# Kernel optimization log

Measured on AMD Instinct MI355X. Metric: run time of the kernel, lower is better.

The kernel has to match this reference:

```python
import jax, jax.numpy as jnp
import numpy as np

N = 30000      # nodes
E = 480000     # edges (avg degree 16)
NF = 4         # n_field
NM = 8         # n_meshfield
H = 128        # hidden_size == latent_size
T = 4          # n_time
DEPTH_MID = 8  # depth-2 middle convs per GCNBlock
EPS = 1e-5     # PyG InstanceNorm eps
DT = 5 * (4.0 / 200)  # = 0.1, hard-coded in forward


def _glorot(k, shape):
    fan_in = shape[-2]
    return (jax.random.uniform(k, shape, jnp.float32, -1.0, 1.0) / np.sqrt(fan_in)).astype(jnp.float32)


def setup_inputs() -> dict:
    key = jax.random.key(0)
    ks = jax.random.split(key, 12)
    inp = {}
    inp['F_0'] = jax.random.normal(ks[0], (N, NF), jnp.float32)
    inp['edge_index'] = jax.random.randint(ks[1], (2, E), 0, N)
    inp['meshfield'] = jax.random.normal(ks[2], (N, NM), jnp.float32)
    inp['n_time'] = T
    # mesh_decriptor GCNBlock params (10 GCNConv layers)
    inp['mesh_W0'] = _glorot(ks[3], (NM, H)); inp['mesh_b0'] = jnp.zeros((H,), jnp.float32)
    inp['mesh_Wh'] = _glorot(ks[4], (DEPTH_MID, H, H)); inp['mesh_bh'] = jnp.zeros((DEPTH_MID, H), jnp.float32)
    inp['mesh_W9'] = _glorot(ks[5], (H, H)); inp['mesh_b9'] = jnp.zeros((H,), jnp.float32)
    # differentiator GCNBlock params; input dim = n_field + latent_size
    din = NF + H
    inp['diff_W0'] = _glorot(ks[6], (din, H)); inp['diff_b0'] = jnp.zeros((H,), jnp.float32)
    inp['diff_Wh'] = _glorot(ks[7], (DEPTH_MID, H, H)); inp['diff_bh'] = jnp.zeros((DEPTH_MID, H), jnp.float32)
    inp['diff_W9'] = _glorot(ks[8], (H, NF)); inp['diff_b9'] = jnp.zeros((NF,), jnp.float32)
    return inp


def _gcn_norm(edge_index, n):
    # PyG GCNConv: add self-loops, sym-normalize D^-1/2 (A+I) D^-1/2
    loops = jnp.arange(n)
    row = jnp.concatenate([edge_index[0], loops])
    col = jnp.concatenate([edge_index[1], loops])
    deg = jax.ops.segment_sum(jnp.ones_like(col, jnp.float32), col, num_segments=n)
    dinv = jnp.where(deg > 0, jax.lax.rsqrt(jnp.maximum(deg, 1.0)), 0.0)
    return row, col, dinv[row] * dinv[col]


def _conv(x, W, b, row, col, enorm, n):
    h = x @ W                                   # [n, out]
    m = h[row] * enorm[:, None]                 # gather + edge normalization
    return jax.ops.segment_sum(m, col, num_segments=n) + b  # scatter-add + bias


def _instance_norm(x):
    # single graph, affine=False: per-channel normalize over nodes
    m = x.mean(axis=0)
    v = x.var(axis=0)
    return (x - m) * jax.lax.rsqrt(v + EPS)


def _gcn_block(x, W0, b0, Wh, bh, W9, b9, row, col, enorm, n):
    x = _conv(x, W0, b0, row, col, enorm, n)
    x = _instance_norm(x)
    def body(c, wb):
        W, b = wb
        return _conv(jax.nn.relu(c), W, b, row, col, enorm, n), None
    x, _ = jax.lax.scan(body, x, (Wh, bh))
    return _conv(x, W9, b9, row, col, enorm, n)


def reference(F_0, edge_index, meshfield, n_time,
              mesh_W0, mesh_b0, mesh_Wh, mesh_bh, mesh_W9, mesh_b9,
              diff_W0, diff_b0, diff_Wh, diff_bh, diff_W9, diff_b9):
    n = F_0.shape[0]
    row, col, enorm = _gcn_norm(edge_index, n)
    mesh = jnp.tanh(_gcn_block(meshfield, mesh_W0, mesh_b0, mesh_Wh, mesh_bh,
                               mesh_W9, mesh_b9, row, col, enorm, n))

    def step(F_cur, _):
        x = jnp.concatenate([F_cur, mesh], axis=1)   # [n, n_field + latent]
        F_dot = jnp.tanh(_gcn_block(x, diff_W0, diff_b0, diff_Wh, diff_bh,
                                    diff_W9, diff_b9, row, col, enorm, n))
        F_next = jnp.tanh(F_cur + F_dot * DT)
        # original: F_current = F_next.detach()
        return jax.lax.stop_gradient(F_next), (F_next, F_dot)

    _, (Fs, F_dots) = jax.lax.scan(step, F_0, None, length=n_time)
    # [T, n, f] -> [n, T, f] to match torch.cat(..., dim=1)
    return jnp.transpose(Fs, (1, 0, 2)), jnp.transpose(F_dots, (1, 0, 2))
```

## Files before the change

kernel.cpp:

```cpp
#include <hip/hip_runtime.h>
#include <math.h>

typedef __attribute__((ext_vector_type(8))) short short8;
typedef __attribute__((ext_vector_type(4))) float f32x4;
typedef unsigned int uint;
typedef unsigned short ushort;

__device__ __forceinline__ ushort f2bf(float f) {
  union { float f; uint u; } v; v.f = f;
  uint u = v.u;
  uint r = (u + 0x7FFFu + ((u >> 16) & 1u)) >> 16;
  return (ushort)r;
}
__device__ __forceinline__ float bflo(uint u) { union { uint u; float f; } v; v.u = u << 16; return v.f; }
__device__ __forceinline__ float bfhi(uint u) { union { uint u; float f; } v; v.u = u & 0xFFFF0000u; return v.f; }
__device__ __forceinline__ uint packbf(float a, float b) { return (uint)f2bf(a) | ((uint)f2bf(b) << 16); }


static __global__ void k_count(const int* __restrict__ col, int* __restrict__ cnt, int E) {
  int e = blockIdx.x * blockDim.x + threadIdx.x;
  if (e < E) atomicAdd(&cnt[col[e]], 1);
}

static __global__ void k_dinv(const int* __restrict__ cnt, float* __restrict__ dinv, int N) {
  int v = blockIdx.x * blockDim.x + threadIdx.x;
  if (v < N) dinv[v] = rsqrtf((float)cnt[v] + 1.0f);
}

static __global__ __launch_bounds__(1024) void k_scan(const int* __restrict__ cnt,
                                                      int* __restrict__ rowptr, int N) {
  const int t = threadIdx.x;
  const int per = (N + 1023) / 1024;
  int lo = t * per, hi = min(lo + per, N);
  if (lo > N) lo = N;
  if (hi < lo) hi = lo;
  int sum = 0;
  for (int i = lo; i < hi; ++i) sum += cnt[i];
  int lane = t & 63, w = t >> 6;
  int v = sum;
#pragma unroll
  for (int d = 1; d < 64; d <<= 1) {
    int u = __shfl_up(v, d, 64);
    if (lane >= d) v += u;
  }
  __shared__ int wsum[16];
  if (lane == 63) wsum[w] = v;
  __syncthreads();
  if (t < 16) {
    int x = wsum[t];
#pragma unroll
    for (int d = 1; d < 16; d <<= 1) {
      int u = __shfl_up(x, d, 64);
      if (t >= d) x += u;
    }
    wsum[t] = x;
  }
  __syncthreads();
  int base = (w ? wsum[w - 1] : 0) + v - sum;
  int run = base;
  for (int i = lo; i < hi; ++i) { rowptr[i] = run; run += cnt[i]; }
  if (t == 1023) rowptr[N] = run;
}

static __global__ void k_fill(const int* __restrict__ row, const int* __restrict__ col,
                              const float* __restrict__ dinv, const int* __restrict__ rowptr,
                              int* __restrict__ fillc, int* __restrict__ csr_src,
                              float* __restrict__ csr_w, int E) {
  int e = blockIdx.x * blockDim.x + threadIdx.x;
  if (e >= E) return;
  int s = row[e], d = col[e];
  int pos = rowptr[d] + atomicAdd(&fillc[d], 1);
  csr_src[pos] = s;
  csr_w[pos] = dinv[s] * dinv[d];
}


static __global__ void k_wprep(const float* __restrict__ W, ushort* __restrict__ Wt,
                               int K, int Kpad, int Nc) {
  int l = blockIdx.y;
  int idx = blockIdx.x * 256 + threadIdx.x;
  if (idx >= Nc * Kpad) return;
  int n = idx / Kpad, k = idx - n * Kpad;
  const float* Wl = W + (size_t)l * K * Nc;
  ushort* Wtl = Wt + (size_t)l * Nc * Kpad;
  Wtl[idx] = (k < K) ? f2bf(Wl[(size_t)k * Nc + n]) : (ushort)0;
}


static __global__ __launch_bounds__(256) void k_gemm16(
    const ushort* __restrict__ A, const ushort* __restrict__ Bt,
    int K, const float* __restrict__ bias,
    float* __restrict__ outF, ushort* __restrict__ outB,
    int M) {
  __shared__ ushort As[128 * 40];
  __shared__ ushort Bs[128 * 40];
  const int tid = threadIdx.x;
  const int lane = tid & 63;
  const int wave = tid >> 6;
  const int wr = wave >> 1, wc = wave & 1;
  const int bm = blockIdx.x * 128;
  const int l15 = lane & 15, lk = lane >> 4;
  const int r0 = tid >> 2, o0 = tid & 3;

  f32x4 acc[4][4];
#pragma unroll
  for (int i = 0; i < 4; ++i)
#pragma unroll
    for (int j = 0; j < 4; ++j) acc[i][j] = (f32x4){0.f, 0.f, 0.f, 0.f};

  for (int k0 = 0; k0 < K; k0 += 32) {
    short8 a0 = *(const short8*)(A + (size_t)(bm + r0) * K + k0 + o0 * 8);
    short8 a1 = *(const short8*)(A + (size_t)(bm + r0 + 64) * K + k0 + o0 * 8);
    short8 b0 = *(const short8*)(Bt + (size_t)r0 * K + k0 + o0 * 8);
    short8 b1 = *(const short8*)(Bt + (size_t)(r0 + 64) * K + k0 + o0 * 8);
    __syncthreads();
    *(short8*)(As + r0 * 40 + o0 * 8) = a0;
    *(short8*)(As + (r0 + 64) * 40 + o0 * 8) = a1;
    *(short8*)(Bs + r0 * 40 + o0 * 8) = b0;
    *(short8*)(Bs + (r0 + 64) * 40 + o0 * 8) = b1;
    __syncthreads();
    short8 af[4], bfr[4];
#pragma unroll
    for (int i = 0; i < 4; ++i) {
      af[i]  = *(const short8*)(As + (wr * 64 + i * 16 + l15) * 40 + lk * 8);
      bfr[i] = *(const short8*)(Bs + (wc * 64 + i * 16 + l15) * 40 + lk * 8);
    }
#pragma unroll
    for (int i = 0; i < 4; ++i)
#pragma unroll
      for (int j = 0; j < 4; ++j)
        acc[i][j] = __builtin_amdgcn_mfma_f32_16x16x32_bf16(af[i], bfr[j], acc[i][j], 0, 0, 0);
  }
#pragma unroll
  for (int i = 0; i < 4; ++i) {
#pragma unroll
    for (int r = 0; r < 4; ++r) {
      int row = bm + wr * 64 + i * 16 + lk * 4 + r;
      if (row >= M) continue;
#pragma unroll
      for (int j = 0; j < 4; ++j) {
        int col = wc * 64 + j * 16 + l15;
        float v = acc[i][j][r] + (bias ? bias[col] : 0.f);
        if (outF) outF[(size_t)row * 128 + col] = v;
        if (outB) outB[(size_t)row * 128 + col] = f2bf(v);
      }
    }
  }
}


static __global__ __launch_bounds__(256) void k_gemm_small(
    const ushort* __restrict__ A, const float* __restrict__ W, float* __restrict__ Y, int M) {
  __shared__ float Ws[512];
  int tid = threadIdx.x;
  for (int i = tid; i < 512; i += 256) Ws[i] = W[i];
  __syncthreads();
  int m = blockIdx.x * 256 + tid;
  if (m >= M) return;
  const uint* a = (const uint*)(A + (size_t)m * 128);
  float a0 = 0, a1 = 0, a2 = 0, a3 = 0;
#pragma unroll 8
  for (int k2 = 0; k2 < 64; ++k2) {
    uint u = a[k2];
    float x0 = bflo(u), x1 = bfhi(u);
    const float* w = Ws + k2 * 8;
    a0 += x0 * w[0] + x1 * w[4];
    a1 += x0 * w[1] + x1 * w[5];
    a2 += x0 * w[2] + x1 * w[6];
    a3 += x0 * w[3] + x1 * w[7];
  }
  float* y = Y + (size_t)m * 4;
  y[0] = a0; y[1] = a1; y[2] = a2; y[3] = a3;
}


static __global__ __launch_bounds__(256) void k_agg16(
    const ushort* __restrict__ Hm, const int* __restrict__ rowptr,
    const int* __restrict__ csr_src, const float* __restrict__ csr_w,
    const float* __restrict__ dinv, const float* __restrict__ bias,
    float* __restrict__ outF,
    ushort* __restrict__ outB, int actB,
    int N) {
  int node = blockIdx.x * 8 + (threadIdx.x >> 5);
  if (node >= N) return;
  int lane = threadIdx.x & 31;
  const uint2* __restrict__ Hu = (const uint2*)Hm;
  float dv = dinv[node];
  float w = dv * dv;
  uint2 su = Hu[(size_t)node * 32 + lane];
  float a0 = w * bflo(su.x), a1 = w * bfhi(su.x);
  float a2 = w * bflo(su.y), a3 = w * bfhi(su.y);
  int s = rowptr[node], e = rowptr[node + 1];
  int i = s;
  for (; i + 8 <= e; i += 8) {
    int s0 = csr_src[i], s1 = csr_src[i + 1], s2 = csr_src[i + 2], s3 = csr_src[i + 3];
    int s4 = csr_src[i + 4], s5 = csr_src[i + 5], s6 = csr_src[i + 6], s7 = csr_src[i + 7];
    float w0 = csr_w[i], w1 = csr_w[i + 1], w2 = csr_w[i + 2], w3 = csr_w[i + 3];
    float w4 = csr_w[i + 4], w5 = csr_w[i + 5], w6 = csr_w[i + 6], w7 = csr_w[i + 7];
    uint2 u0 = Hu[(size_t)s0 * 32 + lane];
    uint2 u1 = Hu[(size_t)s1 * 32 + lane];
    uint2 u2 = Hu[(size_t)s2 * 32 + lane];
    uint2 u3 = Hu[(size_t)s3 * 32 + lane];
    uint2 u4 = Hu[(size_t)s4 * 32 + lane];
    uint2 u5 = Hu[(size_t)s5 * 32 + lane];
    uint2 u6 = Hu[(size_t)s6 * 32 + lane];
    uint2 u7 = Hu[(size_t)s7 * 32 + lane];
    a0 += w0 * bflo(u0.x) + w1 * bflo(u1.x) + w2 * bflo(u2.x) + w3 * bflo(u3.x)
        + w4 * bflo(u4.x) + w5 * bflo(u5.x) + w6 * bflo(u6.x) + w7 * bflo(u7.x);
    a1 += w0 * bfhi(u0.x) + w1 * bfhi(u1.x) + w2 * bfhi(u2.x) + w3 * bfhi(u3.x)
        + w4 * bfhi(u4.x) + w5 * bfhi(u5.x) + w6 * bfhi(u6.x) + w7 * bfhi(u7.x);
    a2 += w0 * bflo(u0.y) + w1 * bflo(u1.y) + w2 * bflo(u2.y) + w3 * bflo(u3.y)
        + w4 * bflo(u4.y) + w5 * bflo(u5.y) + w6 * bflo(u6.y) + w7 * bflo(u7.y);
    a3 += w0 * bfhi(u0.y) + w1 * bfhi(u1.y) + w2 * bfhi(u2.y) + w3 * bfhi(u3.y)
        + w4 * bfhi(u4.y) + w5 * bfhi(u5.y) + w6 * bfhi(u6.y) + w7 * bfhi(u7.y);
  }
  for (; i + 4 <= e; i += 4) {
    int s0 = csr_src[i], s1 = csr_src[i + 1], s2 = csr_src[i + 2], s3 = csr_src[i + 3];
    float w0 = csr_w[i], w1 = csr_w[i + 1], w2 = csr_w[i + 2], w3 = csr_w[i + 3];
    uint2 u0 = Hu[(size_t)s0 * 32 + lane];
    uint2 u1 = Hu[(size_t)s1 * 32 + lane];
    uint2 u2 = Hu[(size_t)s2 * 32 + lane];
    uint2 u3 = Hu[(size_t)s3 * 32 + lane];
    a0 += w0 * bflo(u0.x) + w1 * bflo(u1.x) + w2 * bflo(u2.x) + w3 * bflo(u3.x);
    a1 += w0 * bfhi(u0.x) + w1 * bfhi(u1.x) + w2 * bfhi(u2.x) + w3 * bfhi(u3.x);
    a2 += w0 * bflo(u0.y) + w1 * bflo(u1.y) + w2 * bflo(u2.y) + w3 * bflo(u3.y);
    a3 += w0 * bfhi(u0.y) + w1 * bfhi(u1.y) + w2 * bfhi(u2.y) + w3 * bfhi(u3.y);
  }
  for (; i < e; ++i) {
    int s0 = csr_src[i];
    float w0 = csr_w[i];
    uint2 u0 = Hu[(size_t)s0 * 32 + lane];
    a0 += w0 * bflo(u0.x);
    a1 += w0 * bfhi(u0.x);
    a2 += w0 * bflo(u0.y);
    a3 += w0 * bfhi(u0.y);
  }
  if (bias) {
    float4 bb = *(const float4*)(bias + lane * 4);
    a0 += bb.x; a1 += bb.y; a2 += bb.z; a3 += bb.w;
  }
  if (outF) {
    *(float4*)(outF + (size_t)node * 128 + lane * 4) = make_float4(a0, a1, a2, a3);
  }
  if (outB) {
    float o0 = a0, o1 = a1, o2 = a2, o3 = a3;
    if (actB == 1) {
      o0 = fmaxf(o0, 0.f); o1 = fmaxf(o1, 0.f); o2 = fmaxf(o2, 0.f); o3 = fmaxf(o3, 0.f);
    } else if (actB == 2) {
      o0 = tanhf(o0); o1 = tanhf(o1); o2 = tanhf(o2); o3 = tanhf(o3);
    }
    uint2 ov;
    ov.x = packbf(o0, o1);
    ov.y = packbf(o2, o3);
    ((uint2*)outB)[(size_t)node * 32 + lane] = ov;
  }
}


static __global__ void k_aggF(const float* __restrict__ F, const int* __restrict__ rowptr,
                              const int* __restrict__ csr_src, const float* __restrict__ csr_w,
                              const float* __restrict__ dinv, ushort* __restrict__ AggF16, int N) {
  int idx = blockIdx.x * blockDim.x + threadIdx.x;
  if (idx >= N * 2) return;
  int v = idx >> 1, pr = idx & 1;
  float dv = dinv[v];
  float2 x = *(const float2*)(F + (size_t)v * 4 + pr * 2);
  float a0 = dv * dv * x.x, a1 = dv * dv * x.y;
  int s = rowptr[v], e = rowptr[v + 1];
  for (int i = s; i < e; ++i) {
    float2 xs = *(const float2*)(F + (size_t)csr_src[i] * 4 + pr * 2);
    float w = csr_w[i];
    a0 += w * xs.x;
    a1 += w * xs.y;
  }
  ((uint*)AggF16)[idx] = packbf(a0, a1);
}


static __global__ void k_concat160(const ushort* __restrict__ AggF16,
                                   const ushort* __restrict__ AggMesh16,
                                   ushort* __restrict__ C160, int N) {
  int idx = blockIdx.x * blockDim.x + threadIdx.x;
  if (idx >= N * 80) return;
  int v = idx / 80, j = idx - v * 80;
  uint val = 0;
  if (j < 2) val = ((const uint*)AggF16)[(size_t)v * 2 + j];
  else if (j < 66) val = ((const uint*)AggMesh16)[(size_t)v * 64 + (j - 2)];
  ((uint*)C160)[idx] = val;
}


static __global__ void k_agg_f32(const float* __restrict__ Hm, float* __restrict__ Y,
                                 const int* __restrict__ rowptr, const int* __restrict__ csr_src,
                                 const float* __restrict__ csr_w, const float* __restrict__ dinv,
                                 const float* __restrict__ bias, int N, int C) {
  int idx = blockIdx.x * blockDim.x + threadIdx.x;
  if (idx >= N * C) return;
  int v = idx / C, c = idx - v * C;
  float dv = dinv[v];
  float acc = dv * dv * Hm[(size_t)v * C + c];
  int s = rowptr[v], e = rowptr[v + 1];
  for (int i = s; i < e; ++i) acc += csr_w[i] * Hm[(size_t)csr_src[i] * C + c];
  Y[idx] = acc + bias[c];
}


static __global__ __launch_bounds__(256) void k_in_part(const float* __restrict__ X,
                                                        float* __restrict__ partial, int N) {
  int tid = threadIdx.x;
  int c4 = (tid & 31) * 4;
  int rsub = tid >> 5;
  int row0 = blockIdx.x * 512 + rsub;
  int rowEnd = min(blockIdx.x * 512 + 512, N);
  float s0 = 0, s1 = 0, s2 = 0, s3 = 0, q0 = 0, q1 = 0, q2 = 0, q3 = 0;
  for (int r = row0; r < rowEnd; r += 8) {
    float4 v = *(const float4*)(X + (size_t)r * 128 + c4);
    s0 += v.x; s1 += v.y; s2 += v.z; s3 += v.w;
    q0 += v.x * v.x; q1 += v.y * v.y; q2 += v.z * v.z; q3 += v.w * v.w;
  }
  __shared__ float sb[8][132], qb[8][132];
  sb[rsub][c4] = s0; sb[rsub][c4 + 1] = s1; sb[rsub][c4 + 2] = s2; sb[rsub][c4 + 3] = s3;
  qb[rsub][c4] = q0; qb[rsub][c4 + 1] = q1; qb[rsub][c4 + 2] = q2; qb[rsub][c4 + 3] = q3;
  __syncthreads();
  if (tid < 128) {
    float ss = 0, qq = 0;
#pragma unroll
    for (int g = 0; g < 8; ++g) { ss += sb[g][tid]; qq += qb[g][tid]; }
    partial[(size_t)blockIdx.x * 256 + tid] = ss;
    partial[(size_t)blockIdx.x * 256 + 128 + tid] = qq;
  }
}

static __global__ void k_in_fin(const float* __restrict__ partial, int NB,
                                float* __restrict__ meanv, float* __restrict__ scalev, int N) {
  int c = threadIdx.x;
  if (c >= 128) return;
  float s = 0, q = 0;
  for (int b = 0; b < NB; ++b) {
    s += partial[(size_t)b * 256 + c];
    q += partial[(size_t)b * 256 + 128 + c];
  }
  float m = s / (float)N;
  float var = q / (float)N - m * m;
  meanv[c] = m;
  scalev[c] = rsqrtf(var + 1e-5f);
}

static __global__ void k_in_apply(const float* __restrict__ X, const float* __restrict__ meanv,
                                  const float* __restrict__ scalev, ushort* __restrict__ outB, int N) {
  int idx = blockIdx.x * blockDim.x + threadIdx.x;
  if (idx >= N * 64) return;
  int c2 = idx & 63;
  float2 x = *(const float2*)(X + (size_t)idx * 2);
  float2 mm = *(const float2*)(meanv + c2 * 2);
  float2 sc = *(const float2*)(scalev + c2 * 2);
  float o0 = fmaxf((x.x - mm.x) * sc.x, 0.f);
  float o1 = fmaxf((x.y - mm.y) * sc.y, 0.f);
  ((uint*)outB)[idx] = packbf(o0, o1);
}


static __global__ void k_cast_mesh0(const float* __restrict__ MF, ushort* __restrict__ C32, int N) {
  int idx = blockIdx.x * blockDim.x + threadIdx.x;
  if (idx >= N * 16) return;
  int v = idx >> 4, c2 = idx & 15;
  int c = c2 * 2;
  float x0 = 0.f, x1 = 0.f;
  if (c < 8) { x0 = MF[v * 8 + c]; x1 = MF[v * 8 + c + 1]; }
  ((uint*)C32)[idx] = packbf(x0, x1);
}

static __global__ void k_copy(const float* __restrict__ A, float* __restrict__ B, int n) {
  int i = blockIdx.x * blockDim.x + threadIdx.x;
  if (i < n) B[i] = A[i];
}

static __global__ void k_step_finish(const float* __restrict__ fdot_pre,
                                     const float* __restrict__ Fcur, float* __restrict__ Fnext,
                                     float* __restrict__ out, int N, int T, int t) {
  int idx = blockIdx.x * blockDim.x + threadIdx.x;
  if (idx >= N * 4) return;
  int v = idx >> 2, f = idx & 3;
  float fd = tanhf(fdot_pre[idx]);
  float fn = tanhf(Fcur[idx] + fd * 0.1f);
  Fnext[idx] = fn;
  out[((size_t)v * T + t) * 4 + f] = fn;
  out[(size_t)N * T * 4 + ((size_t)v * T + t) * 4 + f] = fd;
}


extern "C" void kernel_launch(void* const* d_in, const int* in_sizes, int n_in,
                              void* d_out, int out_size, void* d_ws, size_t ws_size,
                              hipStream_t stream) {
  const float* F0        = (const float*)d_in[0];
  const int*   ei        = (const int*)d_in[1];
  const float* meshfield = (const float*)d_in[2];
  const float* mesh_W0 = (const float*)d_in[4];
  const float* mesh_b0 = (const float*)d_in[5];
  const float* mesh_Wh = (const float*)d_in[6];
  const float* mesh_bh = (const float*)d_in[7];
  const float* mesh_W9 = (const float*)d_in[8];
  const float* mesh_b9 = (const float*)d_in[9];
  const float* diff_W0 = (const float*)d_in[10];
  const float* diff_b0 = (const float*)d_in[11];
  const float* diff_Wh = (const float*)d_in[12];
  const float* diff_bh = (const float*)d_in[13];
  const float* diff_W9 = (const float*)d_in[14];
  const float* diff_b9 = (const float*)d_in[15];

  const int N = in_sizes[0] / 4;
  const int E = in_sizes[1] / 2;
  const int H = in_sizes[5];
  const int T = out_size / (N * 4 * 2);
  const int DEPTH = in_sizes[7] / H;
  const int Mpad = (N + 127) / 128 * 128;
  const int NB_IN = (N + 511) / 512;

  const int* erow = ei;
  const int* ecol = ei + E;

  char* p = (char*)d_ws;
  auto alloc = [&](size_t bytes) { char* r = p; p += (bytes + 255) & ~(size_t)255; return r; };
  float* dinv     = (float*)alloc((size_t)N * 4);
  float* X        = (float*)alloc((size_t)N * H * 4);
  ushort* C32     = (ushort*)alloc((size_t)Mpad * 32 * 2);
  ushort* C160    = (ushort*)alloc((size_t)Mpad * 160 * 2);
  ushort* X16a    = (ushort*)alloc((size_t)Mpad * 128 * 2);
  ushort* X16b    = (ushort*)alloc((size_t)Mpad * 128 * 2);
  ushort* Msg16   = (ushort*)alloc((size_t)Mpad * 128 * 2);
  ushort* meshL16 = (ushort*)alloc((size_t)Mpad * 128 * 2);
  ushort* AggM16  = (ushort*)alloc((size_t)Mpad * 128 * 2);
  ushort* AggF16  = (ushort*)alloc((size_t)Mpad * 4 * 2);
  float* msg4     = (float*)alloc((size_t)N * 4 * 4);
  float* fdotp    = (float*)alloc((size_t)N * 4 * 4);
  float* fcur0    = (float*)alloc((size_t)N * 4 * 4);
  float* fcur1    = (float*)alloc((size_t)N * 4 * 4);
  float* partial  = (float*)alloc((size_t)NB_IN * 256 * 4);
  float* meanv    = (float*)alloc(128 * 4);
  float* scalev   = (float*)alloc(128 * 4);
  ushort* W0t_m   = (ushort*)alloc((size_t)128 * 32 * 2);
  ushort* Wht_m   = (ushort*)alloc((size_t)DEPTH * 128 * 128 * 2);
  ushort* W9t_m   = (ushort*)alloc((size_t)128 * 128 * 2);
  ushort* W0t_d   = (ushort*)alloc((size_t)128 * 160 * 2);
  ushort* Wht_d   = (ushort*)alloc((size_t)DEPTH * 128 * 128 * 2);
  float* csr_w    = (float*)alloc((size_t)E * 4);
  int* cnt        = (int*)alloc((size_t)N * 4);
  int* rowptr     = (int*)alloc((size_t)(N + 1) * 4);
  int* fillc      = (int*)alloc((size_t)N * 4);
  int* csr_src    = (int*)alloc((size_t)E * 4);

  {
    dim3 g0((128 * 32 + 255) / 256, 1);
    k_wprep<<<g0, 256, 0, stream>>>(mesh_W0, W0t_m, 8, 32, 128);
    dim3 gh((128 * 128 + 255) / 256, DEPTH);
    k_wprep<<<gh, 256, 0, stream>>>(mesh_Wh, Wht_m, 128, 128, 128);
    dim3 g9((128 * 128 + 255) / 256, 1);
    k_wprep<<<g9, 256, 0, stream>>>(mesh_W9, W9t_m, 128, 128, 128);
    dim3 gd((128 * 160 + 255) / 256, 1);
    k_wprep<<<gd, 256, 0, stream>>>(diff_W0, W0t_d, 132, 160, 128);
    k_wprep<<<gh, 256, 0, stream>>>(diff_Wh, Wht_d, 128, 128, 128);
  }

  hipMemsetAsync(cnt, 0, (size_t)N * 4, stream);
  hipMemsetAsync(fillc, 0, (size_t)N * 4, stream);
  k_count<<<(E + 255) / 256, 256, 0, stream>>>(ecol, cnt, E);
  k_dinv<<<(N + 255) / 256, 256, 0, stream>>>(cnt, dinv, N);
  k_scan<<<1, 1024, 0, stream>>>(cnt, rowptr, N);
  k_fill<<<(E + 255) / 256, 256, 0, stream>>>(erow, ecol, dinv, rowptr, fillc, csr_src, csr_w, E);

  auto gemm = [&](const ushort* A, const ushort* Bt, int K, const float* bias,
                  float* oF, ushort* oB) {
    k_gemm16<<<Mpad / 128, 256, 0, stream>>>(A, Bt, K, bias, oF, oB, N);
  };
  auto agg = [&](const ushort* Hm, const float* bias, float* oF, ushort* oB, int actB) {
    k_agg16<<<(N + 7) / 8, 256, 0, stream>>>(Hm, rowptr, csr_src, csr_w, dinv, bias,
                                             oF, oB, actB, N);
  };
  auto instnorm = [&]() {
    k_in_part<<<NB_IN, 256, 0, stream>>>(X, partial, N);
    k_in_fin<<<1, 128, 0, stream>>>(partial, NB_IN, meanv, scalev, N);
    k_in_apply<<<(N * 64 + 255) / 256, 256, 0, stream>>>(X, meanv, scalev, X16a, N);
  };

  k_cast_mesh0<<<(N * 16 + 255) / 256, 256, 0, stream>>>(meshfield, C32, N);
  gemm(C32, W0t_m, 32, nullptr, nullptr, Msg16);
  agg(Msg16, mesh_b0, X, nullptr, 0);
  instnorm();
  {
    ushort* cur = X16a; ushort* nxt = X16b;
    for (int i = 0; i < DEPTH; ++i) {
      gemm(cur, Wht_m + (size_t)i * 128 * 128, 128, nullptr, nullptr, Msg16);
      agg(Msg16, mesh_bh + (size_t)i * H, nullptr, nxt, (i < DEPTH - 1) ? 1 : 0);
      ushort* tmp = cur; cur = nxt; nxt = tmp;
    }
    gemm(cur, W9t_m, 128, nullptr, nullptr, Msg16);
    agg(Msg16, mesh_b9, nullptr, meshL16, 2 );
  }
  agg(meshL16, nullptr, nullptr, AggM16, 0);

  k_copy<<<(N * 4 + 255) / 256, 256, 0, stream>>>(F0, fcur0, N * 4);
  float* fc = fcur0;
  float* fn = fcur1;
  float* out = (float*)d_out;

  for (int t = 0; t < T; ++t) {
    k_aggF<<<(N * 2 + 255) / 256, 256, 0, stream>>>(fc, rowptr, csr_src, csr_w, dinv, AggF16, N);
    k_concat160<<<(N * 80 + 255) / 256, 256, 0, stream>>>(AggF16, AggM16, C160, N);
    gemm(C160, W0t_d, 160, diff_b0, X, nullptr);
    instnorm();
    ushort* cur = X16a; ushort* nxt = X16b;
    for (int i = 0; i < DEPTH; ++i) {
      gemm(cur, Wht_d + (size_t)i * 128 * 128, 128, nullptr, nullptr, Msg16);
      agg(Msg16, diff_bh + (size_t)i * H, nullptr, nxt, (i < DEPTH - 1) ? 1 : 0);
      ushort* tmp = cur; cur = nxt; nxt = tmp;
    }
    k_gemm_small<<<(N + 255) / 256, 256, 0, stream>>>(cur, diff_W9, msg4, N);
    k_agg_f32<<<(N * 4 + 255) / 256, 256, 0, stream>>>(msg4, fdotp, rowptr, csr_src, csr_w,
                                                       dinv, diff_b9, N, 4);
    k_step_finish<<<(N * 4 + 255) / 256, 256, 0, stream>>>(fdotp, fc, fn, out, N, T, t);
    float* tmp = fc; fc = fn; fn = tmp;
  }
}
```

Measured before the change: 2.182 ms.

## Fuse instance-norm stats into GEMM epilogue, widen aggregation loads, drop concat kernel

The first differentiator GEMM now accumulates per-column sum and sum-of-squares into a global stats buffer with atomics, replacing the separate partial-reduction and finalize kernels. The apply kernel computes mean and scale itself. The aggregation kernel switches to 16 lanes per node with 16-byte loads and drops the 4-edge unrolled path. The per-step concat kernel is removed: the static mesh part of C160 is built once and aggF writes its columns directly. Float atomics make the statistics nondeterministic in summation order and add a memset per step.

```diff
diff --git a/kernel.cpp b/kernel.cpp
--- a/kernel.cpp
+++ b/kernel.cpp
@@ -91,6 +91,7 @@
     const ushort* __restrict__ A, const ushort* __restrict__ Bt,
     int K, const float* __restrict__ bias,
     float* __restrict__ outF, ushort* __restrict__ outB,
+    float* __restrict__ statac,
     int M) {
   __shared__ ushort As[128 * 40];
   __shared__ ushort Bs[128 * 40];
@@ -144,6 +145,35 @@
         if (outF) outF[(size_t)row * 128 + col] = v;
         if (outB) outB[(size_t)row * 128 + col] = f2bf(v);
       }
+    }
+  }
+  if (statac) {
+    __syncthreads();
+    float* sums = (float*)As;
+    for (int ii = tid; ii < 256; ii += 256) sums[ii] = 0.f;
+    __syncthreads();
+#pragma unroll
+    for (int j = 0; j < 4; ++j) {
+      int col = wc * 64 + j * 16 + l15;
+      float s = 0.f, q = 0.f;
+#pragma unroll
+      for (int i = 0; i < 4; ++i) {
+#pragma unroll
+        for (int r = 0; r < 4; ++r) {
+          int row = bm + wr * 64 + i * 16 + lk * 4 + r;
+          if (row < M) {
+            float v = acc[i][j][r] + (bias ? bias[col] : 0.f);
+            s += v; q += v * v;
+          }
+        }
+      }
+      atomicAdd(&sums[col], s);
+      atomicAdd(&sums[128 + col], q);
+    }
+    __syncthreads();
+    if (tid < 128) {
+      atomicAdd(&statac[tid], sums[tid]);
+      atomicAdd(&statac[128 + tid], sums[128 + tid]);
     }
   }
 }
@@ -181,15 +211,17 @@
     float* __restrict__ outF,
     ushort* __restrict__ outB, int actB,
     int N) {
-  int node = blockIdx.x * 8 + (threadIdx.x >> 5);
+  int node = blockIdx.x * 16 + (threadIdx.x >> 4);
   if (node >= N) return;
-  int lane = threadIdx.x & 31;
-  const uint2* __restrict__ Hu = (const uint2*)Hm;
+  int lane = threadIdx.x & 15;
+  const uint4* __restrict__ Hq = (const uint4*)Hm;
   float dv = dinv[node];
   float w = dv * dv;
-  uint2 su = Hu[(size_t)node * 32 + lane];
+  uint4 su = Hq[(size_t)node * 16 + lane];
   float a0 = w * bflo(su.x), a1 = w * bfhi(su.x);
   float a2 = w * bflo(su.y), a3 = w * bfhi(su.y);
+  float a4 = w * bflo(su.z), a5 = w * bfhi(su.z);
+  float a6 = w * bflo(su.w), a7 = w * bfhi(su.w);
   int s = rowptr[node], e = rowptr[node + 1];
   int i = s;
   for (; i + 8 <= e; i += 8) {
@@ -197,14 +229,14 @@
     int s4 = csr_src[i + 4], s5 = csr_src[i + 5], s6 = csr_src[i + 6], s7 = csr_src[i + 7];
     float w0 = csr_w[i], w1 = csr_w[i + 1], w2 = csr_w[i + 2], w3 = csr_w[i + 3];
     float w4 = csr_w[i + 4], w5 = csr_w[i + 5], w6 = csr_w[i + 6], w7 = csr_w[i + 7];
-    uint2 u0 = Hu[(size_t)s0 * 32 + lane];
-    uint2 u1 = Hu[(size_t)s1 * 32 + lane];
-    uint2 u2 = Hu[(size_t)s2 * 32 + lane];
-    uint2 u3 = Hu[(size_t)s3 * 32 + lane];
-    uint2 u4 = Hu[(size_t)s4 * 32 + lane];
-    uint2 u5 = Hu[(size_t)s5 * 32 + lane];
-    uint2 u6 = Hu[(size_t)s6 * 32 + lane];
-    uint2 u7 = Hu[(size_t)s7 * 32 + lane];
+    uint4 u0 = Hq[(size_t)s0 * 16 + lane];
+    uint4 u1 = Hq[(size_t)s1 * 16 + lane];
+    uint4 u2 = Hq[(size_t)s2 * 16 + lane];
+    uint4 u3 = Hq[(size_t)s3 * 16 + lane];
+    uint4 u4 = Hq[(size_t)s4 * 16 + lane];
+    uint4 u5 = Hq[(size_t)s5 * 16 + lane];
+    uint4 u6 = Hq[(size_t)s6 * 16 + lane];
+    uint4 u7 = Hq[(size_t)s7 * 16 + lane];
     a0 += w0 * bflo(u0.x) + w1 * bflo(u1.x) + w2 * bflo(u2.x) + w3 * bflo(u3.x)
         + w4 * bflo(u4.x) + w5 * bflo(u5.x) + w6 * bflo(u6.x) + w7 * bflo(u7.x);
     a1 += w0 * bfhi(u0.x) + w1 * bfhi(u1.x) + w2 * bfhi(u2.x) + w3 * bfhi(u3.x)
@@ -213,53 +245,54 @@
         + w4 * bflo(u4.y) + w5 * bflo(u5.y) + w6 * bflo(u6.y) + w7 * bflo(u7.y);
     a3 += w0 * bfhi(u0.y) + w1 * bfhi(u1.y) + w2 * bfhi(u2.y) + w3 * bfhi(u3.y)
         + w4 * bfhi(u4.y) + w5 * bfhi(u5.y) + w6 * bfhi(u6.y) + w7 * bfhi(u7.y);
-  }
-  for (; i + 4 <= e; i += 4) {
-    int s0 = csr_src[i], s1 = csr_src[i + 1], s2 = csr_src[i + 2], s3 = csr_src[i + 3];
-    float w0 = csr_w[i], w1 = csr_w[i + 1], w2 = csr_w[i + 2], w3 = csr_w[i + 3];
-    uint2 u0 = Hu[(size_t)s0 * 32 + lane];
-    uint2 u1 = Hu[(size_t)s1 * 32 + lane];
-    uint2 u2 = Hu[(size_t)s2 * 32 + lane];
-    uint2 u3 = Hu[(size_t)s3 * 32 + lane];
-    a0 += w0 * bflo(u0.x) + w1 * bflo(u1.x) + w2 * bflo(u2.x) + w3 * bflo(u3.x);
-    a1 += w0 * bfhi(u0.x) + w1 * bfhi(u1.x) + w2 * bfhi(u2.x) + w3 * bfhi(u3.x);
-    a2 += w0 * bflo(u0.y) + w1 * bflo(u1.y) + w2 * bflo(u2.y) + w3 * bflo(u3.y);
-    a3 += w0 * bfhi(u0.y) + w1 * bfhi(u1.y) + w2 * bfhi(u2.y) + w3 * bfhi(u3.y);
+    a4 += w0 * bflo(u0.z) + w1 * bflo(u1.z) + w2 * bflo(u2.z) + w3 * bflo(u3.z)
+        + w4 * bflo(u4.z) + w5 * bflo(u5.z) + w6 * bflo(u6.z) + w7 * bflo(u7.z);
+    a5 += w0 * bfhi(u0.z) + w1 * bfhi(u1.z) + w2 * bfhi(u2.z) + w3 * bfhi(u3.z)
+        + w4 * bfhi(u4.z) + w5 * bfhi(u5.z) + w6 * bfhi(u6.z) + w7 * bfhi(u7.z);
+    a6 += w0 * bflo(u0.w) + w1 * bflo(u1.w) + w2 * bflo(u2.w) + w3 * bflo(u3.w)
+        + w4 * bflo(u4.w) + w5 * bflo(u5.w) + w6 * bflo(u6.w) + w7 * bflo(u7.w);
+    a7 += w0 * bfhi(u0.w) + w1 * bfhi(u1.w) + w2 * bfhi(u2.w) + w3 * bfhi(u3.w)
+        + w4 * bfhi(u4.w) + w5 * bfhi(u5.w) + w6 * bfhi(u6.w) + w7 * bfhi(u7.w);
   }
   for (; i < e; ++i) {
     int s0 = csr_src[i];
     float w0 = csr_w[i];
-    uint2 u0 = Hu[(size_t)s0 * 32 + lane];
-    a0 += w0 * bflo(u0.x);
-    a1 += w0 * bfhi(u0.x);
-    a2 += w0 * bflo(u0.y);
-    a3 += w0 * bfhi(u0.y);
+    uint4 u0 = Hq[(size_t)s0 * 16 + lane];
+    a0 += w0 * bflo(u0.x); a1 += w0 * bfhi(u0.x);
+    a2 += w0 * bflo(u0.y); a3 += w0 * bfhi(u0.y);
+    a4 += w0 * bflo(u0.z); a5 += w0 * bfhi(u0.z);
+    a6 += w0 * bflo(u0.w); a7 += w0 * bfhi(u0.w);
   }
   if (bias) {
-    float4 bb = *(const float4*)(bias + lane * 4);
-    a0 += bb.x; a1 += bb.y; a2 += bb.z; a3 += bb.w;
+    float4 b0 = *(const float4*)(bias + lane * 8);
+    float4 b1 = *(const float4*)(bias + lane * 8 + 4);
+    a0 += b0.x; a1 += b0.y; a2 += b0.z; a3 += b0.w;
+    a4 += b1.x; a5 += b1.y; a6 += b1.z; a7 += b1.w;
   }
   if (outF) {
-    *(float4*)(outF + (size_t)node * 128 + lane * 4) = make_float4(a0, a1, a2, a3);
+    *(float4*)(outF + (size_t)node * 128 + lane * 8)     = make_float4(a0, a1, a2, a3);
+    *(float4*)(outF + (size_t)node * 128 + lane * 8 + 4) = make_float4(a4, a5, a6, a7);
   }
   if (outB) {
-    float o0 = a0, o1 = a1, o2 = a2, o3 = a3;
+    float o0 = a0, o1 = a1, o2 = a2, o3 = a3, o4 = a4, o5 = a5, o6 = a6, o7 = a7;
     if (actB == 1) {
       o0 = fmaxf(o0, 0.f); o1 = fmaxf(o1, 0.f); o2 = fmaxf(o2, 0.f); o3 = fmaxf(o3, 0.f);
+      o4 = fmaxf(o4, 0.f); o5 = fmaxf(o5, 0.f); o6 = fmaxf(o6, 0.f); o7 = fmaxf(o7, 0.f);
     } else if (actB == 2) {
       o0 = tanhf(o0); o1 = tanhf(o1); o2 = tanhf(o2); o3 = tanhf(o3);
-    }
-    uint2 ov;
-    ov.x = packbf(o0, o1);
-    ov.y = packbf(o2, o3);
-    ((uint2*)outB)[(size_t)node * 32 + lane] = ov;
+      o4 = tanhf(o4); o5 = tanhf(o5); o6 = tanhf(o6); o7 = tanhf(o7);
+    }
+    uint4 ov;
+    ov.x = packbf(o0, o1); ov.y = packbf(o2, o3);
+    ov.z = packbf(o4, o5); ov.w = packbf(o6, o7);
+    ((uint4*)outB)[(size_t)node * 16 + lane] = ov;
   }
 }
 
 
 static __global__ void k_aggF(const float* __restrict__ F, const int* __restrict__ rowptr,
                               const int* __restrict__ csr_src, const float* __restrict__ csr_w,
-                              const float* __restrict__ dinv, ushort* __restrict__ AggF16, int N) {
+                              const float* __restrict__ dinv, ushort* __restrict__ C160, int N) {
   int idx = blockIdx.x * blockDim.x + threadIdx.x;
   if (idx >= N * 2) return;
   int v = idx >> 1, pr = idx & 1;
@@ -273,19 +306,17 @@
     a0 += w * xs.x;
     a1 += w * xs.y;
   }
-  ((uint*)AggF16)[idx] = packbf(a0, a1);
-}
-
-
-static __global__ void k_concat160(const ushort* __restrict__ AggF16,
-                                   const ushort* __restrict__ AggMesh16,
-                                   ushort* __restrict__ C160, int N) {
+  ((uint*)C160)[(size_t)v * 80 + pr] = packbf(a0, a1);
+}
+
+
+static __global__ void k_buildC160(const ushort* __restrict__ AggMesh16,
+                                   ushort* __restrict__ C160, int N, int Mpad) {
   int idx = blockIdx.x * blockDim.x + threadIdx.x;
-  if (idx >= N * 80) return;
+  if (idx >= Mpad * 80) return;
   int v = idx / 80, j = idx - v * 80;
   uint val = 0;
-  if (j < 2) val = ((const uint*)AggF16)[(size_t)v * 2 + j];
-  else if (j < 66) val = ((const uint*)AggMesh16)[(size_t)v * 64 + (j - 2)];
+  if (j >= 2 && j < 66 && v < N) val = ((const uint*)AggMesh16)[(size_t)v * 64 + (j - 2)];
   ((uint*)C160)[idx] = val;
 }
 
@@ -306,7 +337,7 @@
 
 
 static __global__ __launch_bounds__(256) void k_in_part(const float* __restrict__ X,
-                                                        float* __restrict__ partial, int N) {
+                                                        float* __restrict__ statac, int N) {
   int tid = threadIdx.x;
   int c4 = (tid & 31) * 4;
   int rsub = tid >> 5;
@@ -326,36 +357,29 @@
     float ss = 0, qq = 0;
 #pragma unroll
     for (int g = 0; g < 8; ++g) { ss += sb[g][tid]; qq += qb[g][tid]; }
-    partial[(size_t)blockIdx.x * 256 + tid] = ss;
-    partial[(size_t)blockIdx.x * 256 + 128 + tid] = qq;
-  }
-}
-
-static __global__ void k_in_fin(const float* __restrict__ partial, int NB,
-                                float* __restrict__ meanv, float* __restrict__ scalev, int N) {
-  int c = threadIdx.x;
-  if (c >= 128) return;
-  float s = 0, q = 0;
-  for (int b = 0; b < NB; ++b) {
-    s += partial[(size_t)b * 256 + c];
-    q += partial[(size_t)b * 256 + 128 + c];
-  }
-  float m = s / (float)N;
-  float var = q / (float)N - m * m;
-  meanv[c] = m;
-  scalev[c] = rsqrtf(var + 1e-5f);
-}
-
-static __global__ void k_in_apply(const float* __restrict__ X, const float* __restrict__ meanv,
-                                  const float* __restrict__ scalev, ushort* __restrict__ outB, int N) {
-  int idx = blockIdx.x * blockDim.x + threadIdx.x;
+    atomicAdd(&statac[tid], ss);
+    atomicAdd(&statac[128 + tid], qq);
+  }
+}
+
+static __global__ __launch_bounds__(256) void k_in_apply(const float* __restrict__ X,
+                                                         const float* __restrict__ statac,
+                                                         ushort* __restrict__ outB, int N) {
+  __shared__ float mv[128], sv[128];
+  int tid = threadIdx.x;
+  if (tid < 128) {
+    float m = statac[tid] / (float)N;
+    float var = statac[128 + tid] / (float)N - m * m;
+    mv[tid] = m;
+    sv[tid] = rsqrtf(var + 1e-5f);
+  }
+  __syncthreads();
+  int idx = blockIdx.x * 256 + tid;
   if (idx >= N * 64) return;
   int c2 = idx & 63;
   float2 x = *(const float2*)(X + (size_t)idx * 2);
-  float2 mm = *(const float2*)(meanv + c2 * 2);
-  float2 sc = *(const float2*)(scalev + c2 * 2);
-  float o0 = fmaxf((x.x - mm.x) * sc.x, 0.f);
-  float o1 = fmaxf((x.y - mm.y) * sc.y, 0.f);
+  float o0 = fmaxf((x.x - mv[c2 * 2]) * sv[c2 * 2], 0.f);
+  float o1 = fmaxf((x.y - mv[c2 * 2 + 1]) * sv[c2 * 2 + 1], 0.f);
   ((uint*)outB)[idx] = packbf(o0, o1);
 }
 
@@ -414,7 +438,6 @@
   const int T = out_size / (N * 4 * 2);
   const int DEPTH = in_sizes[7] / H;
   const int Mpad = (N + 127) / 128 * 128;
-  const int NB_IN = (N + 511) / 512;
 
   const int* erow = ei;
   const int* ecol = ei + E;
@@ -430,14 +453,11 @@
   ushort* Msg16   = (ushort*)alloc((size_t)Mpad * 128 * 2);
   ushort* meshL16 = (ushort*)alloc((size_t)Mpad * 128 * 2);
   ushort* AggM16  = (ushort*)alloc((size_t)Mpad * 128 * 2);
-  ushort* AggF16  = (ushort*)alloc((size_t)Mpad * 4 * 2);
   float* msg4     = (float*)alloc((size_t)N * 4 * 4);
   float* fdotp    = (float*)alloc((size_t)N * 4 * 4);
   float* fcur0    = (float*)alloc((size_t)N * 4 * 4);
   float* fcur1    = (float*)alloc((size_t)N * 4 * 4);
-  float* partial  = (float*)alloc((size_t)NB_IN * 256 * 4);
-  float* meanv    = (float*)alloc(128 * 4);
-  float* scalev   = (float*)alloc(128 * 4);
+  float* statac   = (float*)alloc(256 * 4);
   ushort* W0t_m   = (ushort*)alloc((size_t)128 * 32 * 2);
   ushort* Wht_m   = (ushort*)alloc((size_t)DEPTH * 128 * 128 * 2);
   ushort* W9t_m   = (ushort*)alloc((size_t)128 * 128 * 2);
@@ -469,34 +489,35 @@
   k_fill<<<(E + 255) / 256, 256, 0, stream>>>(erow, ecol, dinv, rowptr, fillc, csr_src, csr_w, E);
 
   auto gemm = [&](const ushort* A, const ushort* Bt, int K, const float* bias,
-                  float* oF, ushort* oB) {
-    k_gemm16<<<Mpad / 128, 256, 0, stream>>>(A, Bt, K, bias, oF, oB, N);
+                  float* oF, ushort* oB, float* st) {
+    k_gemm16<<<Mpad / 128, 256, 0, stream>>>(A, Bt, K, bias, oF, oB, st, N);
   };
   auto agg = [&](const ushort* Hm, const float* bias, float* oF, ushort* oB, int actB) {
-    k_agg16<<<(N + 7) / 8, 256, 0, stream>>>(Hm, rowptr, csr_src, csr_w, dinv, bias,
-                                             oF, oB, actB, N);
+    k_agg16<<<(N + 15) / 16, 256, 0, stream>>>(Hm, rowptr, csr_src, csr_w, dinv, bias,
+                                               oF, oB, actB, N);
   };
-  auto instnorm = [&]() {
-    k_in_part<<<NB_IN, 256, 0, stream>>>(X, partial, N);
-    k_in_fin<<<1, 128, 0, stream>>>(partial, NB_IN, meanv, scalev, N);
-    k_in_apply<<<(N * 64 + 255) / 256, 256, 0, stream>>>(X, meanv, scalev, X16a, N);
+  auto in_apply = [&]() {
+    k_in_apply<<<(N * 64 + 255) / 256, 256, 0, stream>>>(X, statac, X16a, N);
   };
 
   k_cast_mesh0<<<(N * 16 + 255) / 256, 256, 0, stream>>>(meshfield, C32, N);
-  gemm(C32, W0t_m, 32, nullptr, nullptr, Msg16);
+  gemm(C32, W0t_m, 32, nullptr, nullptr, Msg16, nullptr);
   agg(Msg16, mesh_b0, X, nullptr, 0);
-  instnorm();
+  hipMemsetAsync(statac, 0, 256 * 4, stream);
+  k_in_part<<<(N + 511) / 512, 256, 0, stream>>>(X, statac, N);
+  in_apply();
   {
     ushort* cur = X16a; ushort* nxt = X16b;
     for (int i = 0; i < DEPTH; ++i) {
-      gemm(cur, Wht_m + (size_t)i * 128 * 128, 128, nullptr, nullptr, Msg16);
+      gemm(cur, Wht_m + (size_t)i * 128 * 128, 128, nullptr, nullptr, Msg16, nullptr);
       agg(Msg16, mesh_bh + (size_t)i * H, nullptr, nxt, (i < DEPTH - 1) ? 1 : 0);
       ushort* tmp = cur; cur = nxt; nxt = tmp;
     }
-    gemm(cur, W9t_m, 128, nullptr, nullptr, Msg16);
+    gemm(cur, W9t_m, 128, nullptr, nullptr, Msg16, nullptr);
     agg(Msg16, mesh_b9, nullptr, meshL16, 2 );
   }
   agg(meshL16, nullptr, nullptr, AggM16, 0);
+  k_buildC160<<<(Mpad * 80 + 255) / 256, 256, 0, stream>>>(AggM16, C160, N, Mpad);
 
   k_copy<<<(N * 4 + 255) / 256, 256, 0, stream>>>(F0, fcur0, N * 4);
   float* fc = fcur0;
@@ -504,13 +525,13 @@
   float* out = (float*)d_out;
 
   for (int t = 0; t < T; ++t) {
-    k_aggF<<<(N * 2 + 255) / 256, 256, 0, stream>>>(fc, rowptr, csr_src, csr_w, dinv, AggF16, N);
-    k_concat160<<<(N * 80 + 255) / 256, 256, 0, stream>>>(AggF16, AggM16, C160, N);
-    gemm(C160, W0t_d, 160, diff_b0, X, nullptr);
-    instnorm();
+    k_aggF<<<(N * 2 + 255) / 256, 256, 0, stream>>>(fc, rowptr, csr_src, csr_w, dinv, C160, N);
+    hipMemsetAsync(statac, 0, 256 * 4, stream);
+    gemm(C160, W0t_d, 160, diff_b0, X, nullptr, statac);
+    in_apply();
     ushort* cur = X16a; ushort* nxt = X16b;
     for (int i = 0; i < DEPTH; ++i) {
-      gemm(cur, Wht_d + (size_t)i * 128 * 128, 128, nullptr, nullptr, Msg16);
+      gemm(cur, Wht_d + (size_t)i * 128 * 128, 128, nullptr, nullptr, Msg16, nullptr);
       agg(Msg16, diff_bh + (size_t)i * H, nullptr, nxt, (i < DEPTH - 1) ? 1 : 0);
       ushort* tmp = cur; cur = nxt; nxt = tmp;
     }
```

After: 2.232 ms. 1.02x slower.
